# Kernel optimization log

Hardware: AMD Instinct MI355X
Metric: run time of the kernel (lower is better)

The kernel has to match this reference:

```python
import jax, jax.numpy as jnp
import numpy as np

B, P, T = 64, 8400, 100


def _corners(b):
    # b: [..., 4] in (cx, cy, w, h) -> (x1, y1, x2, y2)
    cx, cy, w, h = b[..., 0], b[..., 1], b[..., 2], b[..., 3]
    return cx - w / 2, cy - h / 2, cx + w / 2, cy + h / 2


def _pairwise_iou(pred_box, tgt_box):
    # pred_box: [B, P, 4], tgt_box: [B, T, 4] -> iou [B, T, P]
    px1, py1, px2, py2 = _corners(pred_box[:, None, :, :])   # [B,1,P]
    tx1, ty1, tx2, ty2 = _corners(tgt_box[:, :, None, :])    # [B,T,1]
    ix1 = jnp.maximum(px1, tx1)
    iy1 = jnp.maximum(py1, ty1)
    ix2 = jnp.minimum(px2, tx2)
    iy2 = jnp.minimum(py2, ty2)
    inter = jnp.maximum(ix2 - ix1, 0.0) * jnp.maximum(iy2 - iy1, 0.0)
    area_p = (px2 - px1) * (py2 - py1)
    area_t = (tx2 - tx1) * (ty2 - ty1)
    return inter / (area_p + area_t - inter + 1e-6)


def setup_inputs() -> dict:
    key = jax.random.key(0)
    k1, k2, k3 = jax.random.split(key, 3)
    predictions = jax.random.uniform(k1, (B, P, 5), dtype=jnp.float32)
    targets = jax.random.uniform(k2, (B, T, 5), dtype=jnp.float32)
    lengths = jax.random.randint(k3, (B,), 0, T, dtype=jnp.int64)
    return {"predictions": predictions, "targets": targets, "lengths": lengths}


def reference(predictions, targets, lengths):
    # predictions: [B, P, 5], targets: [B, T, 5], lengths: [B]
    iou = _pairwise_iou(predictions[..., 1:], targets[..., 1:])  # [B, T, P]
    # strict '>' in original keeps first max; argmax also returns first occurrence
    best_idx = jnp.argmax(iou, axis=-1)                          # [B, T]
    matched = jnp.take_along_axis(predictions, best_idx[..., None], axis=1)  # [B, T, 5]
    sq = jnp.sum((matched - targets) ** 2, axis=-1)              # [B, T]
    valid = jnp.arange(targets.shape[1]) < lengths[:, None]      # [B, T]
    loss = jnp.sum(jnp.where(valid, sq, 0.0)) / predictions.shape[0]
    return loss
```

## Files before the change

kernel.cpp:

```cpp
#include <hip/hip_runtime.h>

#define BB 64
#define PP 8400
#define TT 100
#define TG 5
#define NGRP (TT / TG)
#define NBLK (BB * NGRP)

__global__ __launch_bounds__(256) void yolo_match_kernel(
    const float* __restrict__ pred,
    const float* __restrict__ tgt,
    const int*   __restrict__ lengths,
    float* __restrict__ ws)
{
#pragma clang fp contract(off)
    const int blkraw = blockIdx.x;
    const int x    = blkraw & 7;
    const int r    = blkraw >> 3;
    const int bhi  = r / NGRP;
    const int grp  = r - bhi * NGRP;
    const int b    = x + 8 * bhi;
    const int t0   = grp * TG;
    const int tid  = threadIdx.x;
    const int lane = tid & 63;
    const int wid  = tid >> 6;

    const float*  pb  = pred + (size_t)b * PP * 5;
    const float4* pb4 = (const float4*)pb;
    const float*  tb  = tgt + ((size_t)b * TT + t0) * 5;

    float tx1[TG], ty1[TG], tx2[TG], ty2[TG], ta[TG];
#pragma unroll
    for (int g = 0; g < TG; ++g) {
        const float tcx = tb[g * 5 + 1], tcy = tb[g * 5 + 2];
        const float tw  = tb[g * 5 + 3], th  = tb[g * 5 + 4];
        tx1[g] = tcx - tw * 0.5f;
        ty1[g] = tcy - th * 0.5f;
        tx2[g] = tcx + tw * 0.5f;
        ty2[g] = tcy + th * 0.5f;
        ta[g]  = (tx2[g] - tx1[g]) * (ty2[g] - ty1[g]);
    }

    float best[TG];
    int   bidx[TG];
#pragma unroll
    for (int g = 0; g < TG; ++g) { best[g] = -1.0f; bidx[g] = 0; }

    for (int g0 = tid; g0 < PP / 8; g0 += 256) {
        float4 q[10];
#pragma unroll
        for (int k = 0; k < 10; ++k) q[k] = pb4[g0 * 10 + k];

        float cxs[8], cys[8], wss[8], hss[8];
#pragma unroll
        for (int h = 0; h < 2; ++h) {
            const float4 v0 = q[5 * h + 0];
            const float4 v1 = q[5 * h + 1];
            const float4 v2 = q[5 * h + 2];
            const float4 v3 = q[5 * h + 3];
            const float4 v4 = q[5 * h + 4];
            cxs[4 * h + 0] = v0.y; cys[4 * h + 0] = v0.z; wss[4 * h + 0] = v0.w; hss[4 * h + 0] = v1.x;
            cxs[4 * h + 1] = v1.z; cys[4 * h + 1] = v1.w; wss[4 * h + 1] = v2.x; hss[4 * h + 1] = v2.y;
            cxs[4 * h + 2] = v2.w; cys[4 * h + 2] = v3.x; wss[4 * h + 2] = v3.y; hss[4 * h + 2] = v3.z;
            cxs[4 * h + 3] = v4.x; cys[4 * h + 3] = v4.y; wss[4 * h + 3] = v4.z; hss[4 * h + 3] = v4.w;
        }

#pragma unroll
        for (int j = 0; j < 8; ++j) {
            const float px1 = cxs[j] - wss[j] * 0.5f;
            const float py1 = cys[j] - hss[j] * 0.5f;
            const float px2 = cxs[j] + wss[j] * 0.5f;
            const float py2 = cys[j] + hss[j] * 0.5f;
            const float area_p = (px2 - px1) * (py2 - py1);
            const int   p = g0 * 8 + j;

#pragma unroll
            for (int g = 0; g < TG; ++g) {
                const float ix1 = fmaxf(px1, tx1[g]);
                const float iy1 = fmaxf(py1, ty1[g]);
                const float ix2 = fminf(px2, tx2[g]);
                const float iy2 = fminf(py2, ty2[g]);
                const float inter = fmaxf(ix2 - ix1, 0.0f) * fmaxf(iy2 - iy1, 0.0f);
                const float denom = ((area_p + ta[g]) - inter) + 1e-6f;
                const float iou   = inter / denom;
                if (iou > best[g]) { best[g] = iou; bidx[g] = p; }
            }
        }
    }

    __shared__ float s_best[4][TG];
    __shared__ int   s_bidx[4][TG];
    __shared__ float s_sq[TG];

#pragma unroll
    for (int g = 0; g < TG; ++g) {
        float bv = best[g];
        int   bi = bidx[g];
        for (int off = 32; off > 0; off >>= 1) {
            const float ob = __shfl_down(bv, off, 64);
            const int   oi = __shfl_down(bi, off, 64);
            if (ob > bv || (ob == bv && oi < bi)) { bv = ob; bi = oi; }
        }
        if (lane == 0) { s_best[wid][g] = bv; s_bidx[wid][g] = bi; }
    }
    __syncthreads();

    if (tid < TG) {
        const int g = tid;
        float bv = s_best[0][g];
        int   bi = s_bidx[0][g];
#pragma unroll
        for (int w = 1; w < 4; ++w) {
            const float ob = s_best[w][g];
            const int   oi = s_bidx[w][g];
            if (ob > bv || (ob == bv && oi < bi)) { bv = ob; bi = oi; }
        }
        const float* mp = pb + bi * 5;
        const float* tp = tb + g * 5;
        float sq = 0.0f;
        for (int k = 0; k < 5; ++k) {
            const float d = mp[k] - tp[k];
            sq += d * d;
        }
        const bool valid = ((t0 + g) < lengths[b]);
        s_sq[g] = valid ? sq : 0.0f;
    }
    __syncthreads();

    if (tid == 0) {
        ws[blkraw] = ((s_sq[0] + s_sq[1]) + (s_sq[2] + s_sq[3])) + s_sq[4];
    }
}

__global__ __launch_bounds__(256) void yolo_reduce_kernel(
    const float* __restrict__ ws,
    float* __restrict__ out)
{
    const int tid = threadIdx.x;
    float s = 0.0f;
    for (int i = tid; i < NBLK; i += 256) s += ws[i];

    __shared__ float sm[256];
    sm[tid] = s;
    __syncthreads();
    for (int off = 128; off > 0; off >>= 1) {
        if (tid < off) sm[tid] += sm[tid + off];
        __syncthreads();
    }
    if (tid == 0) out[0] = sm[0] / (float)BB;
}

extern "C" void kernel_launch(void* const* d_in, const int* in_sizes, int n_in,
                              void* d_out, int out_size, void* d_ws, size_t ws_size,
                              hipStream_t stream) {
    const float* pred    = (const float*)d_in[0];
    const float* tgt     = (const float*)d_in[1];
    const int*   lengths = (const int*)d_in[2];
    float* out = (float*)d_out;
    float* ws  = (float*)d_ws;

    yolo_match_kernel<<<NBLK, 256, 0, stream>>>(pred, tgt, lengths, ws);
    yolo_reduce_kernel<<<1, 256, 0, stream>>>(ws, out);
}
```

Measured before the change: 105.5 us.

## Split prediction range across two blocks per target group and merge in finish kernel

Each (batch, target-group) block is split into two blocks, each scanning half of the 8400 predictions and writing its partial best IoU and index to workspace. A new single-block finish kernel merges the two halves, keeping the first half on ties, then gathers the matched prediction, computes the masked squared error and reduces to the loss. This doubles the block count, from 1280 to 2560, to raise occupancy and shorten per-block serial work. The cost is more workspace traffic and a heavier serial finish kernel.

```diff
diff --git a/kernel.cpp b/kernel.cpp
--- a/kernel.cpp
+++ b/kernel.cpp
@@ -5,20 +5,26 @@
 #define TT 100
 #define TG 5
 #define NGRP (TT / TG)
-#define NBLK (BB * NGRP)
+#define NSPLIT 2
+#define NBLK (BB * NGRP * NSPLIT)
+#define NGROUPS8 (PP / 8)
+#define GRPH (NGROUPS8 / NSPLIT)
+#define NE (BB * TT)
 
 __global__ __launch_bounds__(256) void yolo_match_kernel(
     const float* __restrict__ pred,
     const float* __restrict__ tgt,
-    const int*   __restrict__ lengths,
-    float* __restrict__ ws)
+    float*       __restrict__ wsbest,
+    int*         __restrict__ wsidx)
 {
 #pragma clang fp contract(off)
     const int blkraw = blockIdx.x;
     const int x    = blkraw & 7;
     const int r    = blkraw >> 3;
-    const int bhi  = r / NGRP;
-    const int grp  = r - bhi * NGRP;
+    const int bhi  = r / (NGRP * NSPLIT);
+    const int rem  = r - bhi * (NGRP * NSPLIT);
+    const int grp  = rem / NSPLIT;
+    const int half = rem - grp * NSPLIT;
     const int b    = x + 8 * bhi;
     const int t0   = grp * TG;
     const int tid  = threadIdx.x;
@@ -46,7 +52,9 @@
 #pragma unroll
     for (int g = 0; g < TG; ++g) { best[g] = -1.0f; bidx[g] = 0; }
 
-    for (int g0 = tid; g0 < PP / 8; g0 += 256) {
+    const int gbeg = half * GRPH;
+    const int gend = gbeg + GRPH;
+    for (int g0 = gbeg + tid; g0 < gend; g0 += 256) {
         float4 q[10];
 #pragma unroll
         for (int k = 0; k < 10; ++k) q[k] = pb4[g0 * 10 + k];
@@ -90,7 +98,6 @@
 
     __shared__ float s_best[4][TG];
     __shared__ int   s_bidx[4][TG];
-    __shared__ float s_sq[TG];
 
 #pragma unroll
     for (int g = 0; g < TG; ++g) {
@@ -115,35 +122,47 @@
             const int   oi = s_bidx[w][g];
             if (ob > bv || (ob == bv && oi < bi)) { bv = ob; bi = oi; }
         }
-        const float* mp = pb + bi * 5;
-        const float* tp = tb + g * 5;
+        const int e = ((b * TT + t0 + g) << 1) | half;
+        wsbest[e] = bv;
+        wsidx[e]  = bi;
+    }
+}
+
+__global__ __launch_bounds__(1024) void yolo_finish_kernel(
+    const float* __restrict__ pred,
+    const float* __restrict__ tgt,
+    const int*   __restrict__ lengths,
+    const float* __restrict__ wsbest,
+    const int*   __restrict__ wsidx,
+    float*       __restrict__ out)
+{
+#pragma clang fp contract(off)
+    const int tid = threadIdx.x;
+    float acc = 0.0f;
+
+    for (int e = tid; e < NE; e += 1024) {
+        const int b = e / TT;
+        const int t = e - b * TT;
+        const float b0 = wsbest[2 * e + 0];
+        const float b1 = wsbest[2 * e + 1];
+        const int   i0 = wsidx[2 * e + 0];
+        const int   i1 = wsidx[2 * e + 1];
+        const int   bi = (b1 > b0) ? i1 : i0;
+
+        const float* mp = pred + ((size_t)b * PP + bi) * 5;
+        const float* tp = tgt  + ((size_t)b * TT + t) * 5;
         float sq = 0.0f;
         for (int k = 0; k < 5; ++k) {
             const float d = mp[k] - tp[k];
             sq += d * d;
         }
-        const bool valid = ((t0 + g) < lengths[b]);
-        s_sq[g] = valid ? sq : 0.0f;
+        acc += (t < lengths[b]) ? sq : 0.0f;
     }
+
+    __shared__ float sm[1024];
+    sm[tid] = acc;
     __syncthreads();
-
-    if (tid == 0) {
-        ws[blkraw] = ((s_sq[0] + s_sq[1]) + (s_sq[2] + s_sq[3])) + s_sq[4];
-    }
-}
-
-__global__ __launch_bounds__(256) void yolo_reduce_kernel(
-    const float* __restrict__ ws,
-    float* __restrict__ out)
-{
-    const int tid = threadIdx.x;
-    float s = 0.0f;
-    for (int i = tid; i < NBLK; i += 256) s += ws[i];
-
-    __shared__ float sm[256];
-    sm[tid] = s;
-    __syncthreads();
-    for (int off = 128; off > 0; off >>= 1) {
+    for (int off = 512; off > 0; off >>= 1) {
         if (tid < off) sm[tid] += sm[tid + off];
         __syncthreads();
     }
@@ -157,8 +176,11 @@
     const float* tgt     = (const float*)d_in[1];
     const int*   lengths = (const int*)d_in[2];
     float* out = (float*)d_out;
-    float* ws  = (float*)d_ws;
 
-    yolo_match_kernel<<<NBLK, 256, 0, stream>>>(pred, tgt, lengths, ws);
-    yolo_reduce_kernel<<<1, 256, 0, stream>>>(ws, out);
+    float* wsbest = (float*)d_ws;
+    int*   wsidx  = (int*)d_ws + NE * NSPLIT;
+
+    yolo_match_kernel<<<NBLK, 256, 0, stream>>>(pred, tgt, wsbest, wsidx);
+    yolo_finish_kernel<<<1, 1024, 0, stream>>>(pred, tgt, lengths,
+                                               wsbest, wsidx, out);
 }
```

After: 119.2 us. +13.0%, slower.
